# Kernel tuning notes

Measured on AMD Instinct MI355X. Metric: run time of the kernel, lower is better.

The kernel has to match this reference:

```python
import jax, jax.numpy as jnp
import numpy as np

EBIT = 8  # exponent word length -> exponent clamped to [-128, 127]
BITS = 8  # wl_activate


def block_quantize(data, bits):
    # push magnitudes away from zero (zeros map to +1e-10), as in the torch code
    data = jnp.where(data >= 0, jnp.maximum(data, 1e-10), jnp.minimum(data, -1e-10))
    # small_block='None' with dim<=4 -> single global max exponent
    max_entry = jnp.max(jnp.abs(data))
    max_exponent = jnp.clip(jnp.floor(jnp.log2(max_entry)),
                            -2.0 ** (EBIT - 1), 2.0 ** (EBIT - 1) - 1)
    i = jnp.round(data * jnp.exp2(-max_exponent + (bits - 2)))  # nearest (half-to-even, same as torch.round)
    i = jnp.clip(i, -2.0 ** (bits - 1), 2.0 ** (bits - 1) - 1)
    return i * jnp.exp2(max_exponent - (bits - 2))


def setup_inputs() -> dict:
    key = jax.random.key(0)
    x = jax.random.normal(key, (16, 2048, 4096), dtype=jnp.float32)
    return {"x": x}


def reference(x):
    return block_quantize(x, BITS)
```

## Files before the change

### kernel.cpp

```cpp
#include <hip/hip_runtime.h>
#include <math.h>

#define GRID 2048
#define BLOCK 256

typedef float nfloat4 __attribute__((ext_vector_type(4)));

__global__ __launch_bounds__(BLOCK) void bq_max_kernel(
    const float4* __restrict__ x, float* __restrict__ partials,
    long long n4, const float* __restrict__ x_scalar, long long n) {
    float m = 0.0f;
    long long stride = (long long)gridDim.x * blockDim.x;
    for (long long i = (long long)blockIdx.x * blockDim.x + threadIdx.x;
         i < n4; i += stride) {
        float4 v = x[i];
        m = fmaxf(m, fmaxf(fmaxf(fabsf(v.x), fabsf(v.y)),
                           fmaxf(fabsf(v.z), fabsf(v.w))));
    }
    if (blockIdx.x == 0 && threadIdx.x == 0) {
        for (long long i = n4 * 4; i < n; ++i) m = fmaxf(m, fabsf(x_scalar[i]));
    }
    #pragma unroll
    for (int off = 32; off > 0; off >>= 1)
        m = fmaxf(m, __shfl_down(m, off, 64));
    __shared__ float smem[BLOCK / 64];
    int lane = threadIdx.x & 63;
    int wave = threadIdx.x >> 6;
    if (lane == 0) smem[wave] = m;
    __syncthreads();
    if (threadIdx.x == 0) {
        float bm = fmaxf(fmaxf(smem[0], smem[1]), fmaxf(smem[2], smem[3]));
        partials[blockIdx.x] = bm;
    }
}

__device__ __forceinline__ float bq_one(float x, float s, float inv) {
    float d = (x >= 0.0f) ? fmaxf(x, 1e-10f) : fminf(x, -1e-10f);
    float i = rintf(d * s);
    i = fminf(fmaxf(i, -128.0f), 127.0f);
    return i * inv;
}

__global__ __launch_bounds__(BLOCK) void bq_quant_kernel(
    const float4* __restrict__ x, nfloat4* __restrict__ out,
    const float* __restrict__ partials, long long n4,
    const float* __restrict__ x_scalar, float* __restrict__ out_scalar,
    long long n) {
    float m = 0.0f;
    #pragma unroll
    for (int k = 0; k < GRID / BLOCK; ++k)
        m = fmaxf(m, partials[threadIdx.x + k * BLOCK]);
    #pragma unroll
    for (int off = 32; off > 0; off >>= 1)
        m = fmaxf(m, __shfl_down(m, off, 64));
    __shared__ float smem[BLOCK / 64];
    __shared__ float sc[2];
    int lane = threadIdx.x & 63;
    int wave = threadIdx.x >> 6;
    if (lane == 0) smem[wave] = m;
    __syncthreads();
    if (threadIdx.x == 0) {
        float bm = fmaxf(fmaxf(smem[0], smem[1]), fmaxf(smem[2], smem[3]));
        bm = fmaxf(bm, 1e-10f);
        int me = ilogbf(bm);
        me = me < -128 ? -128 : (me > 127 ? 127 : me);
        sc[0] = ldexpf(1.0f, 6 - me);
        sc[1] = ldexpf(1.0f, me - 6);
    }
    __syncthreads();
    float s = sc[0], inv = sc[1];

    long long stride = (long long)gridDim.x * blockDim.x;
    long long base = (long long)blockIdx.x * blockDim.x + threadIdx.x;
    long long iters = (n4 - base + stride - 1) / stride;
    for (long long it = iters - 1; it >= 0; --it) {
        long long i = base + it * stride;
        float4 v = x[i];
        nfloat4 r;
        r.x = bq_one(v.x, s, inv);
        r.y = bq_one(v.y, s, inv);
        r.z = bq_one(v.z, s, inv);
        r.w = bq_one(v.w, s, inv);
        __builtin_nontemporal_store(r, &out[i]);
    }
    if (blockIdx.x == 0 && threadIdx.x == 0) {
        for (long long i = n4 * 4; i < n; ++i)
            out_scalar[i] = bq_one(x_scalar[i], s, inv);
    }
}

extern "C" void kernel_launch(void* const* d_in, const int* in_sizes, int n_in,
                              void* d_out, int out_size, void* d_ws, size_t ws_size,
                              hipStream_t stream) {
    const float* x = (const float*)d_in[0];
    float* out = (float*)d_out;
    long long n = (long long)in_sizes[0];
    long long n4 = n / 4;
    float* partials = (float*)d_ws;

    bq_max_kernel<<<GRID, BLOCK, 0, stream>>>(
        (const float4*)x, partials, n4, x, n);
    bq_quant_kernel<<<GRID, BLOCK, 0, stream>>>(
        (const float4*)x, (nfloat4*)out, partials, n4, x, out, n);
}
```

Before: 932.8 us.

## Speculate max exponent from input sample, quantize in one pass, fix up on mismatch

Replaces the full max-reduction pass with a small pass over the first 8M floats (2M float4) to guess the global max exponent. The main kernel then quantizes with the guessed scale while computing the true max. A fixup kernel requantizes everything only if the true exponent differs from the guess. This saves a full read of the input in the common case. It relies on the sample usually holding the max exponent, which holds for Gaussian test data, and it stays correct in general because of the fixup.

```diff
diff --git a/kernel.cpp b/kernel.cpp
--- a/kernel.cpp
+++ b/kernel.cpp
@@ -3,35 +3,29 @@
 
 #define GRID 2048
 #define BLOCK 256
+#define SGRID 128
+#define SAMPLE_F4 (2LL * 1024 * 1024)
 
 typedef float nfloat4 __attribute__((ext_vector_type(4)));
 
-__global__ __launch_bounds__(BLOCK) void bq_max_kernel(
-    const float4* __restrict__ x, float* __restrict__ partials,
-    long long n4, const float* __restrict__ x_scalar, long long n) {
-    float m = 0.0f;
-    long long stride = (long long)gridDim.x * blockDim.x;
-    for (long long i = (long long)blockIdx.x * blockDim.x + threadIdx.x;
-         i < n4; i += stride) {
-        float4 v = x[i];
-        m = fmaxf(m, fmaxf(fmaxf(fabsf(v.x), fabsf(v.y)),
-                           fmaxf(fabsf(v.z), fabsf(v.w))));
-    }
-    if (blockIdx.x == 0 && threadIdx.x == 0) {
-        for (long long i = n4 * 4; i < n; ++i) m = fmaxf(m, fabsf(x_scalar[i]));
-    }
+__device__ __forceinline__ float block_reduce_max(float m) {
     #pragma unroll
     for (int off = 32; off > 0; off >>= 1)
         m = fmaxf(m, __shfl_down(m, off, 64));
     __shared__ float smem[BLOCK / 64];
-    int lane = threadIdx.x & 63;
-    int wave = threadIdx.x >> 6;
-    if (lane == 0) smem[wave] = m;
     __syncthreads();
-    if (threadIdx.x == 0) {
-        float bm = fmaxf(fmaxf(smem[0], smem[1]), fmaxf(smem[2], smem[3]));
-        partials[blockIdx.x] = bm;
-    }
+    if ((threadIdx.x & 63) == 0) smem[threadIdx.x >> 6] = m;
+    __syncthreads();
+    return fmaxf(fmaxf(smem[0], smem[1]), fmaxf(smem[2], smem[3]));
+}
+
+__device__ __forceinline__ void bq_scales(float bm, int* me_out, float* s, float* inv) {
+    bm = fmaxf(bm, 1e-10f);
+    int me = ilogbf(bm);
+    me = me < -128 ? -128 : (me > 127 ? 127 : me);
+    *me_out = me;
+    *s   = ldexpf(1.0f, 6 - me);
+    *inv = ldexpf(1.0f, me - 6);
 }
 
 __device__ __forceinline__ float bq_one(float x, float s, float inv) {
@@ -41,40 +35,79 @@
     return i * inv;
 }
 
-__global__ __launch_bounds__(BLOCK) void bq_quant_kernel(
+__global__ __launch_bounds__(BLOCK) void bq_smax_kernel(
+    const float4* __restrict__ x, float* __restrict__ spart, long long n4) {
+    long long limit = n4 < SAMPLE_F4 ? n4 : SAMPLE_F4;
+    float m = 0.0f;
+    long long stride = (long long)gridDim.x * blockDim.x;
+    for (long long i = (long long)blockIdx.x * blockDim.x + threadIdx.x;
+         i < limit; i += stride) {
+        float4 v = x[i];
+        m = fmaxf(m, fmaxf(fmaxf(fabsf(v.x), fabsf(v.y)),
+                           fmaxf(fabsf(v.z), fabsf(v.w))));
+    }
+    float bm = block_reduce_max(m);
+    if (threadIdx.x == 0) spart[blockIdx.x] = bm;
+}
+
+__global__ __launch_bounds__(BLOCK) void bq_specquant_kernel(
     const float4* __restrict__ x, nfloat4* __restrict__ out,
-    const float* __restrict__ partials, long long n4,
-    const float* __restrict__ x_scalar, float* __restrict__ out_scalar,
-    long long n) {
+    float* __restrict__ partials, const float* __restrict__ spart,
+    long long n4, const float* __restrict__ x_scalar,
+    float* __restrict__ out_scalar, long long n) {
+    float sm0 = spart[threadIdx.x & (SGRID - 1)];
+    float smax = block_reduce_max(sm0);
+    int me_spec; float s, inv;
+    bq_scales(smax, &me_spec, &s, &inv);
+
+    float m = 0.0f;
+    long long stride = (long long)gridDim.x * blockDim.x;
+    for (long long i = (long long)blockIdx.x * blockDim.x + threadIdx.x;
+         i < n4; i += stride) {
+        float4 v = x[i];
+        m = fmaxf(m, fmaxf(fmaxf(fabsf(v.x), fabsf(v.y)),
+                           fmaxf(fabsf(v.z), fabsf(v.w))));
+        nfloat4 r;
+        r.x = bq_one(v.x, s, inv);
+        r.y = bq_one(v.y, s, inv);
+        r.z = bq_one(v.z, s, inv);
+        r.w = bq_one(v.w, s, inv);
+        __builtin_nontemporal_store(r, &out[i]);
+    }
+    if (blockIdx.x == 0 && threadIdx.x == 0) {
+        for (long long i = n4 * 4; i < n; ++i) {
+            float xv = x_scalar[i];
+            m = fmaxf(m, fabsf(xv));
+            out_scalar[i] = bq_one(xv, s, inv);
+        }
+    }
+    float bm = block_reduce_max(m);
+    if (threadIdx.x == 0) partials[blockIdx.x] = bm;
+}
+
+__global__ __launch_bounds__(BLOCK) void bq_fixup_kernel(
+    const float4* __restrict__ x, nfloat4* __restrict__ out,
+    const float* __restrict__ partials, const float* __restrict__ spart,
+    long long n4, const float* __restrict__ x_scalar,
+    float* __restrict__ out_scalar, long long n) {
     float m = 0.0f;
     #pragma unroll
     for (int k = 0; k < GRID / BLOCK; ++k)
         m = fmaxf(m, partials[threadIdx.x + k * BLOCK]);
-    #pragma unroll
-    for (int off = 32; off > 0; off >>= 1)
-        m = fmaxf(m, __shfl_down(m, off, 64));
-    __shared__ float smem[BLOCK / 64];
-    __shared__ float sc[2];
-    int lane = threadIdx.x & 63;
-    int wave = threadIdx.x >> 6;
-    if (lane == 0) smem[wave] = m;
-    __syncthreads();
-    if (threadIdx.x == 0) {
-        float bm = fmaxf(fmaxf(smem[0], smem[1]), fmaxf(smem[2], smem[3]));
-        bm = fmaxf(bm, 1e-10f);
-        int me = ilogbf(bm);
-        me = me < -128 ? -128 : (me > 127 ? 127 : me);
-        sc[0] = ldexpf(1.0f, 6 - me);
-        sc[1] = ldexpf(1.0f, me - 6);
-    }
-    __syncthreads();
-    float s = sc[0], inv = sc[1];
+    float gm = block_reduce_max(m);
+    int me_g; float s, inv;
+    bq_scales(gm, &me_g, &s, &inv);
+
+    float sm0 = spart[threadIdx.x & (SGRID - 1)];
+    float smax = block_reduce_max(sm0);
+    int me_spec; float s_u, inv_u;
+    bq_scales(smax, &me_spec, &s_u, &inv_u);
+
+    if (me_g == me_spec) return;
 
     long long stride = (long long)gridDim.x * blockDim.x;
-    long long base = (long long)blockIdx.x * blockDim.x + threadIdx.x;
-    long long iters = (n4 - base + stride - 1) / stride;
-    for (long long it = iters - 1; it >= 0; --it) {
-        long long i = base + it * stride;
+    for (long long i = (long long)blockIdx.x * blockDim.x + threadIdx.x;
+         i < n4; i += stride) {
         float4 v = x[i];
         nfloat4 r;
         r.x = bq_one(v.x, s, inv);
@@ -97,9 +130,11 @@
     long long n = (long long)in_sizes[0];
     long long n4 = n / 4;
     float* partials = (float*)d_ws;
+    float* spart = partials + GRID;
 
-    bq_max_kernel<<<GRID, BLOCK, 0, stream>>>(
-        (const float4*)x, partials, n4, x, n);
-    bq_quant_kernel<<<GRID, BLOCK, 0, stream>>>(
-        (const float4*)x, (nfloat4*)out, partials, n4, x, out, n);
+    bq_smax_kernel<<<SGRID, BLOCK, 0, stream>>>((const float4*)x, spart, n4);
+    bq_specquant_kernel<<<GRID, BLOCK, 0, stream>>>(
+        (const float4*)x, (nfloat4*)out, partials, spart, n4, x, out, n);
+    bq_fixup_kernel<<<GRID, BLOCK, 0, stream>>>(
+        (const float4*)x, (nfloat4*)out, partials, spart, n4, x, out, n);
 }
```

Result: faster. 868.4 us (-6.9%).
